# Performance work log

Measured on AMD Instinct MI355X. Metric: run time of the kernel, lower is better.

The kernel has to match this reference:

```python
import jax, jax.numpy as jnp
import numpy as np
import math

D_HEAD = 64
D_MODEL = 1024
N_HEADS = D_MODEL // D_HEAD
MAX_TOKENS = 2048
BATCH = 4
SEQ = 2048


def setup_inputs() -> dict:
    key = jax.random.key(0)
    k1, k2, k3, k4, k5 = jax.random.split(key, 5)
    residual_stream = jax.random.normal(k1, (BATCH, SEQ, D_MODEL), dtype=jnp.float32)
    # kaiming_normal_ (fan_in = d_model for [head, d_model, d_head] with default mode)
    std_qkv = math.sqrt(2.0 / D_MODEL)
    weight_query = jax.random.normal(k2, (N_HEADS, D_MODEL, D_HEAD), dtype=jnp.float32) * std_qkv
    weight_key = jax.random.normal(k3, (N_HEADS, D_MODEL, D_HEAD), dtype=jnp.float32) * std_qkv
    weight_value = jax.random.normal(k4, (N_HEADS, D_MODEL, D_HEAD), dtype=jnp.float32) * std_qkv
    # xavier_normal_ for [d_model, d_model]
    std_out = math.sqrt(2.0 / (D_MODEL + D_MODEL))
    weight_out = jax.random.normal(k5, (D_MODEL, D_MODEL), dtype=jnp.float32) * std_out
    return {
        "residual_stream": residual_stream,
        "weight_query": weight_query,
        "weight_key": weight_key,
        "weight_value": weight_value,
        "weight_out": weight_out,
    }


def reference(residual_stream, weight_query, weight_key, weight_value, weight_out):
    # residual_stream: [b, s, m]; weights: [h, m, d]
    q = jnp.einsum("bsm,hmd->bhsd", residual_stream, weight_query)
    k = jnp.einsum("bsm,hmd->bhsd", residual_stream, weight_key)
    v = jnp.einsum("bsm,hmd->bhsd", residual_stream, weight_value)
    scores = jnp.einsum("bhqd,bhkd->bhqk", q, k) / math.sqrt(D_HEAD)  # [b,h,s,s]
    n = scores.shape[-1]
    causal = jnp.tril(jnp.ones((n, n), dtype=bool))
    scores = jnp.where(causal, scores, -jnp.inf)
    attn = jax.nn.softmax(scores, axis=-1)
    out = jnp.einsum("bhqk,bhkd->bhqd", attn, v)  # [b,h,s,d]
    b, h, s, d = out.shape
    concat = out.transpose(0, 2, 1, 3).reshape(b, s, h * d)  # [b,s,m]
    return jnp.einsum("bsm,mn->bsn", concat, weight_out)
```

## Files before the change

### kernel.cpp

```cpp
#include <hip/hip_runtime.h>
#include <hip/hip_bf16.h>
#include <math.h>

#define BATCH 4
#define SEQ   2048
#define DM    1024
#define NH    16
#define DH    64

#define QSCALE 0.1803368801111204f

typedef __bf16 bf16x8 __attribute__((ext_vector_type(8)));
typedef __bf16 bf16x4 __attribute__((ext_vector_type(4)));
typedef float  f32x4  __attribute__((ext_vector_type(4)));

typedef const __attribute__((address_space(1))) unsigned int guint;
typedef __attribute__((address_space(3)))       unsigned int luint;

__device__ __forceinline__ void async16(const __bf16* g, __bf16* l) {
    __builtin_amdgcn_global_load_lds((guint*)g, (luint*)l, 16, 0, 0);
}

__device__ __forceinline__ float fast_exp2(float x) {
#if __has_builtin(__builtin_amdgcn_exp2f)
    return __builtin_amdgcn_exp2f(x);
#else
    float r; asm("v_exp_f32 %0, %1" : "=v"(r) : "v"(x)); return r;
#endif
}
__device__ __forceinline__ float fast_rcp(float x) {
#if __has_builtin(__builtin_amdgcn_rcpf)
    return __builtin_amdgcn_rcpf(x);
#else
    float r; asm("v_rcp_f32 %0, %1" : "=v"(r) : "v"(x)); return r;
#endif
}

__device__ __forceinline__ bf16x8 load8f(const float* __restrict__ base, size_t idx) {
    const float4 a = *(const float4*)(base + idx);
    const float4 b = *(const float4*)(base + idx + 4);
    bf16x8 r;
    r[0] = (__bf16)a.x; r[1] = (__bf16)a.y; r[2] = (__bf16)a.z; r[3] = (__bf16)a.w;
    r[4] = (__bf16)b.x; r[5] = (__bf16)b.y; r[6] = (__bf16)b.z; r[7] = (__bf16)b.w;
    return r;
}

__global__ __launch_bounds__(256)
void xconv_kernel(const float* __restrict__ X, __bf16* __restrict__ Xb)
{
    size_t idx = ((size_t)blockIdx.x * 256 + threadIdx.x) * 8;
    *(bf16x8*)&Xb[idx] = load8f(X, idx);
}

__global__ __launch_bounds__(256)
void wtrans_kernel(const float* __restrict__ src, __bf16* __restrict__ dst,
                   int K, int N)
{
    const int k0 = blockIdx.x * 64;
    const int n0 = blockIdx.y * 64;
    src += (size_t)blockIdx.z * K * N;
    dst += (size_t)blockIdx.z * K * N;

    __shared__ __bf16 T[64][65];
    const int t = threadIdx.x;

#pragma unroll
    for (int i = 0; i < 4; ++i) {
        int row = i * 16 + (t >> 4);
        int col = (t & 15) * 4;
        float4 v = *(const float4*)&src[(size_t)(k0 + row) * N + n0 + col];
        T[col + 0][row] = (__bf16)v.x;
        T[col + 1][row] = (__bf16)v.y;
        T[col + 2][row] = (__bf16)v.z;
        T[col + 3][row] = (__bf16)v.w;
    }
    __syncthreads();
#pragma unroll
    for (int i = 0; i < 4; ++i) {
        int n  = i * 16 + (t >> 4);
        int kc = (t & 15) * 4;
        bf16x4 v;
        v[0] = T[n][kc + 0]; v[1] = T[n][kc + 1];
        v[2] = T[n][kc + 2]; v[3] = T[n][kc + 3];
        *(bf16x4*)&dst[(size_t)(n0 + n) * K + k0 + kc] = v;
    }
}

__global__ __launch_bounds__(256)
void qkv_kernel(const __bf16* __restrict__ Xb,
                const __bf16* __restrict__ Wqt,
                const __bf16* __restrict__ Wkt,
                const __bf16* __restrict__ Wvt,
                __bf16* __restrict__ Qo,
                __bf16* __restrict__ Ko,
                __bf16* __restrict__ Vto)
{
    const int rowTile = blockIdx.x;
    const int h       = blockIdx.y;
    const size_t woff = (size_t)h * DH * DM;

    __shared__ __align__(16) __bf16 As[128 * 32];
    __shared__ __align__(16) __bf16 Bq[64 * 32];
    __shared__ __align__(16) __bf16 Bk[64 * 32];
    __shared__ __align__(16) __bf16 Bv[64 * 32];

    const int t    = threadIdx.x;
    const int wave = t >> 6;
    const int lane = t & 63;
    const int l15  = lane & 15;
    const int quad = lane >> 4;

    f32x4 aq[2][4], ak[2][4], av[2][4];
#pragma unroll
    for (int s = 0; s < 2; ++s)
#pragma unroll
        for (int i = 0; i < 4; ++i) {
            aq[s][i] = (f32x4){0.f, 0.f, 0.f, 0.f};
            ak[s][i] = (f32x4){0.f, 0.f, 0.f, 0.f};
            av[s][i] = (f32x4){0.f, 0.f, 0.f, 0.f};
        }

    const int r0 = rowTile * 128;
    const int lrow = lane >> 2;
    const int lcol = (lane & 3) * 8;

    for (int k0 = 0; k0 < DM; k0 += 32) {
        __syncthreads();
#pragma unroll
        for (int c = 0; c < 2; ++c) {
            const int rb = wave * 32 + c * 16;
            async16(&Xb[(size_t)(r0 + rb + lrow) * DM + k0 + lcol], &As[rb * 32]);
        }
        {
            const int rb = wave * 16;
            async16(&Wqt[woff + (size_t)(rb + lrow) * DM + k0 + lcol], &Bq[rb * 32]);
            async16(&Wkt[woff + (size_t)(rb + lrow) * DM + k0 + lcol], &Bk[rb * 32]);
            async16(&Wvt[woff + (size_t)(rb + lrow) * DM + k0 + lcol], &Bv[rb * 32]);
        }
        __syncthreads();

        bf16x8 a0 = *(const bf16x8*)&As[(wave * 16 + l15) * 32 + quad * 8];
        bf16x8 a1 = *(const bf16x8*)&As[(64 + wave * 16 + l15) * 32 + quad * 8];
#pragma unroll
        for (int ct = 0; ct < 4; ++ct) {
            bf16x8 bq = *(const bf16x8*)&Bq[(ct * 16 + l15) * 32 + quad * 8];
            aq[0][ct] = __builtin_amdgcn_mfma_f32_16x16x32_bf16(a0, bq, aq[0][ct], 0, 0, 0);
            aq[1][ct] = __builtin_amdgcn_mfma_f32_16x16x32_bf16(a1, bq, aq[1][ct], 0, 0, 0);
            bf16x8 bk = *(const bf16x8*)&Bk[(ct * 16 + l15) * 32 + quad * 8];
            ak[0][ct] = __builtin_amdgcn_mfma_f32_16x16x32_bf16(a0, bk, ak[0][ct], 0, 0, 0);
            ak[1][ct] = __builtin_amdgcn_mfma_f32_16x16x32_bf16(a1, bk, ak[1][ct], 0, 0, 0);
            bf16x8 bv = *(const bf16x8*)&Bv[(ct * 16 + l15) * 32 + quad * 8];
            av[0][ct] = __builtin_amdgcn_mfma_f32_16x16x32_bf16(a0, bv, av[0][ct], 0, 0, 0);
            av[1][ct] = __builtin_amdgcn_mfma_f32_16x16x32_bf16(a1, bv, av[1][ct], 0, 0, 0);
        }
    }

#pragma unroll
    for (int st = 0; st < 2; ++st) {
        const int rbase = r0 + st * 64 + wave * 16 + quad * 4;
        const int b = rbase >> 11;
        const int s = rbase & (SEQ - 1);
        const size_t bh = (size_t)(b * NH + h);
#pragma unroll
        for (int ct = 0; ct < 4; ++ct) {
            const int d = ct * 16 + l15;
#pragma unroll
            for (int reg = 0; reg < 4; ++reg) {
                Qo[(bh * SEQ + s + reg) * DH + d] = (__bf16)(aq[st][ct][reg] * QSCALE);
                Ko[(bh * SEQ + s + reg) * DH + d] = (__bf16)ak[st][ct][reg];
            }
            bf16x4 vv;
            vv[0] = (__bf16)av[st][ct][0]; vv[1] = (__bf16)av[st][ct][1];
            vv[2] = (__bf16)av[st][ct][2]; vv[3] = (__bf16)av[st][ct][3];
            *(bf16x4*)&Vto[(bh * DH + d) * SEQ + s] = vv;
        }
    }
}

__global__ __launch_bounds__(256)
void attn_kernel(const __bf16* __restrict__ Q,
                 const __bf16* __restrict__ K,
                 const __bf16* __restrict__ Vt,
                 __bf16* __restrict__ Cat)
{
    const int x   = blockIdx.x;
    const int qtA = x;
    const int qtB = 31 - x;
    const int bh  = blockIdx.y;
    const int b   = bh >> 4;
    const int h   = bh & 15;

    const __bf16* Qg  = Q  + (size_t)bh * SEQ * DH;
    const __bf16* Kg  = K  + (size_t)bh * SEQ * DH;
    const __bf16* Vtg = Vt + (size_t)bh * DH * SEQ;

    __shared__ __align__(16) __bf16 Ks[64 * 72];
    __shared__ __align__(16) __bf16 Vs[64 * 72];
    __shared__ __align__(16) __bf16 Ps[64 * 72];

    const int t    = threadIdx.x;
    const int wave = t >> 6;
    const int lane = t & 63;
    const int l15  = lane & 15;
    const int quad = lane >> 4;

    bf16x8 qfA[2], qfB[2];
    {
        const size_t rA = (size_t)(qtA * 64 + wave * 16 + l15);
        qfA[0] = *(const bf16x8*)&Qg[rA * DH + quad * 8];
        qfA[1] = *(const bf16x8*)&Qg[rA * DH + 32 + quad * 8];
        const size_t rB = (size_t)(qtB * 64 + wave * 16 + l15);
        qfB[0] = *(const bf16x8*)&Qg[rB * DH + quad * 8];
        qfB[1] = *(const bf16x8*)&Qg[rB * DH + 32 + quad * 8];
    }

    bf16x8 ones;
#pragma unroll
    for (int j = 0; j < 8; ++j) ones[j] = (__bf16)1.0f;

    f32x4 oA[4], oB[4], olA, olB;
#pragma unroll
    for (int ct = 0; ct < 4; ++ct) {
        oA[ct] = (f32x4){0.f, 0.f, 0.f, 0.f};
        oB[ct] = (f32x4){0.f, 0.f, 0.f, 0.f};
    }
    olA = (f32x4){0.f, 0.f, 0.f, 0.f};
    olB = (f32x4){0.f, 0.f, 0.f, 0.f};

    const int srow0 = t >> 3;
    const int scol  = (t & 7) * 8;
    bf16x8 kreg[2], vreg[2];
#pragma unroll
    for (int i = 0; i < 2; ++i) {
        int row = srow0 + i * 32;
        kreg[i] = *(const bf16x8*)&Kg[(size_t)row * DH + scol];
        vreg[i] = *(const bf16x8*)&Vtg[(size_t)row * SEQ + scol];
    }

    auto half_step = [&](const bf16x8* qf, f32x4* o, f32x4& ol, bool diag) {
        f32x4 sc[4];
#pragma unroll
        for (int ct = 0; ct < 4; ++ct) {
            sc[ct] = (f32x4){0.f, 0.f, 0.f, 0.f};
            bf16x8 b0 = *(const bf16x8*)&Ks[(ct * 16 + l15) * 72 + quad * 8];
            sc[ct] = __builtin_amdgcn_mfma_f32_16x16x32_bf16(qf[0], b0, sc[ct], 0, 0, 0);
            bf16x8 b1 = *(const bf16x8*)&Ks[(ct * 16 + l15) * 72 + 32 + quad * 8];
            sc[ct] = __builtin_amdgcn_mfma_f32_16x16x32_bf16(qf[1], b1, sc[ct], 0, 0, 0);
        }
        if (diag) {
#pragma unroll
            for (int ct = 0; ct < 4; ++ct)
#pragma unroll
                for (int r = 0; r < 4; ++r) {
                    int qr = wave * 16 + quad * 4 + r;
                    int kc = ct * 16 + l15;
                    if (kc > qr) sc[ct][r] = -INFINITY;
                }
        }
#pragma unroll
        for (int ct = 0; ct < 4; ++ct)
#pragma unroll
            for (int r = 0; r < 4; ++r)
                sc[ct][r] = fast_exp2(sc[ct][r]);

#pragma unroll
        for (int ct = 0; ct < 4; ++ct)
#pragma unroll
            for (int r = 0; r < 4; ++r)
                Ps[(wave * 16 + quad * 4 + r) * 72 + ct * 16 + l15] =
                    (__bf16)sc[ct][r];

        bf16x8 af0 = *(const bf16x8*)&Ps[(wave * 16 + l15) * 72 + quad * 8];
        bf16x8 af1 = *(const bf16x8*)&Ps[(wave * 16 + l15) * 72 + 32 + quad * 8];

#pragma unroll
        for (int ct = 0; ct < 4; ++ct) {
            bf16x8 v0 = *(const bf16x8*)&Vs[(ct * 16 + l15) * 72 + quad * 8];
            o[ct] = __builtin_amdgcn_mfma_f32_16x16x32_bf16(af0, v0, o[ct], 0, 0, 0);
            bf16x8 v1 = *(const bf16x8*)&Vs[(ct * 16 + l15) * 72 + 32 + quad * 8];
            o[ct] = __builtin_amdgcn_mfma_f32_16x16x32_bf16(af1, v1, o[ct], 0, 0, 0);
        }
        ol = __builtin_amdgcn_mfma_f32_16x16x32_bf16(af0, ones, ol, 0, 0, 0);
        ol = __builtin_amdgcn_mfma_f32_16x16x32_bf16(af1, ones, ol, 0, 0, 0);
    };

    for (int kt = 0; kt <= qtB; ++kt) {
        __syncthreads();
#pragma unroll
        for (int i = 0; i < 2; ++i) {
            int row = srow0 + i * 32;
            *(bf16x8*)&Ks[row * 72 + scol] = kreg[i];
            *(bf16x8*)&Vs[row * 72 + scol] = vreg[i];
        }
        __syncthreads();

        {
            const int kvn = (kt < qtB ? kt + 1 : kt) * 64;
#pragma unroll
            for (int i = 0; i < 2; ++i) {
                int row = srow0 + i * 32;
                kreg[i] = *(const bf16x8*)&Kg[(size_t)(kvn + row) * DH + scol];
                vreg[i] = *(const bf16x8*)&Vtg[(size_t)row * SEQ + kvn + scol];
            }
        }

        half_step(qfB, oB, olB, kt == qtB);
        if (kt <= qtA)
            half_step(qfA, oA, olA, kt == qtA);
    }

#pragma unroll
    for (int ct = 0; ct < 4; ++ct)
#pragma unroll
        for (int r = 0; r < 4; ++r) {
            int rr = wave * 16 + quad * 4 + r;
            int sA = qtA * 64 + rr;
            int sB = qtB * 64 + rr;
            Cat[((size_t)(b * SEQ + sA)) * DM + h * DH + ct * 16 + l15] =
                (__bf16)(oA[ct][r] * fast_rcp(olA[r]));
            Cat[((size_t)(b * SEQ + sB)) * DM + h * DH + ct * 16 + l15] =
                (__bf16)(oB[ct][r] * fast_rcp(olB[r]));
        }
}

__global__ __launch_bounds__(256)
void oproj_kernel(const __bf16* __restrict__ A,
                  const __bf16* __restrict__ Wot,
                  float* __restrict__ C)
{
    const int rowTile = blockIdx.x;
    const int colTile = blockIdx.y;
    const int r0 = rowTile * 128;
    const int n0 = colTile * 128;

    __shared__ __align__(16) __bf16 As[128 * 32];
    __shared__ __align__(16) __bf16 Bs[128 * 32];

    const int t    = threadIdx.x;
    const int wave = t >> 6;
    const int lane = t & 63;
    const int l15  = lane & 15;
    const int quad = lane >> 4;

    f32x4 acc[2][8];
#pragma unroll
    for (int s = 0; s < 2; ++s)
#pragma unroll
        for (int i = 0; i < 8; ++i) acc[s][i] = (f32x4){0.f, 0.f, 0.f, 0.f};

    const int lrow = lane >> 2;
    const int lcol = (lane & 3) * 8;

    for (int k0 = 0; k0 < DM; k0 += 32) {
        __syncthreads();
#pragma unroll
        for (int c = 0; c < 2; ++c) {
            const int rb = wave * 32 + c * 16;
            async16(&A  [(size_t)(r0 + rb + lrow) * DM + k0 + lcol], &As[rb * 32]);
            async16(&Wot[(size_t)(n0 + rb + lrow) * DM + k0 + lcol], &Bs[rb * 32]);
        }
        __syncthreads();

        bf16x8 a0 = *(const bf16x8*)&As[(wave * 16 + l15) * 32 + quad * 8];
        bf16x8 a1 = *(const bf16x8*)&As[(64 + wave * 16 + l15) * 32 + quad * 8];
#pragma unroll
        for (int ct = 0; ct < 8; ++ct) {
            bf16x8 bb = *(const bf16x8*)&Bs[(ct * 16 + l15) * 32 + quad * 8];
            acc[0][ct] = __builtin_amdgcn_mfma_f32_16x16x32_bf16(a0, bb, acc[0][ct], 0, 0, 0);
            acc[1][ct] = __builtin_amdgcn_mfma_f32_16x16x32_bf16(a1, bb, acc[1][ct], 0, 0, 0);
        }
    }

#pragma unroll
    for (int st = 0; st < 2; ++st)
#pragma unroll
        for (int ct = 0; ct < 8; ++ct)
#pragma unroll
            for (int reg = 0; reg < 4; ++reg) {
                int r = r0 + st * 64 + wave * 16 + quad * 4 + reg;
                int n = n0 + ct * 16 + l15;
                C[(size_t)r * DM + n] = acc[st][ct][reg];
            }
}

extern "C" void kernel_launch(void* const* d_in, const int* in_sizes, int n_in,
                              void* d_out, int out_size, void* d_ws, size_t ws_size,
                              hipStream_t stream)
{
    (void)in_sizes; (void)n_in; (void)out_size; (void)ws_size;
    const float* X  = (const float*)d_in[0];
    const float* Wq = (const float*)d_in[1];
    const float* Wk = (const float*)d_in[2];
    const float* Wv = (const float*)d_in[3];
    const float* Wo = (const float*)d_in[4];
    float* out = (float*)d_out;

    char* ws = (char*)d_ws;
    const size_t wqkv_b = (size_t)NH * DM * DH * sizeof(__bf16);
    const size_t wo_b   = (size_t)DM * DM * sizeof(__bf16);
    const size_t big_b  = (size_t)BATCH * NH * SEQ * DH * sizeof(__bf16);
    __bf16* Wqt = (__bf16*)(ws);
    __bf16* Wkt = (__bf16*)(ws + wqkv_b);
    __bf16* Wvt = (__bf16*)(ws + 2 * wqkv_b);
    __bf16* Wot = (__bf16*)(ws + 3 * wqkv_b);
    __bf16* Qb  = (__bf16*)(ws + 3 * wqkv_b + wo_b);
    __bf16* Kb  = (__bf16*)(ws + 3 * wqkv_b + wo_b + big_b);
    __bf16* Vtb = (__bf16*)(ws + 3 * wqkv_b + wo_b + 2 * big_b);
    __bf16* Cat = (__bf16*)(ws + 3 * wqkv_b + wo_b + 3 * big_b);
    __bf16* Xb  = (__bf16*)(ws + 3 * wqkv_b + wo_b + 4 * big_b);

    xconv_kernel<<<dim3(4096), 256, 0, stream>>>(X, Xb);
    wtrans_kernel<<<dim3(16, 1, 16), 256, 0, stream>>>(Wq, Wqt, DM, DH);
    wtrans_kernel<<<dim3(16, 1, 16), 256, 0, stream>>>(Wk, Wkt, DM, DH);
    wtrans_kernel<<<dim3(16, 1, 16), 256, 0, stream>>>(Wv, Wvt, DM, DH);
    wtrans_kernel<<<dim3(16, 16, 1), 256, 0, stream>>>(Wo, Wot, DM, DM);
    qkv_kernel<<<dim3(64, 16), 256, 0, stream>>>(Xb, Wqt, Wkt, Wvt, Qb, Kb, Vtb);
    attn_kernel<<<dim3(16, 64), 256, 0, stream>>>(Qb, Kb, Vtb, Cat);
    oproj_kernel<<<dim3(64, 8), 256, 0, stream>>>(Cat, Wot, out);
}
```

Before: 281.6 us.

## Interleave both query tiles' attention steps and merge QKV weight transposes

The attention inner loop now computes scores for both query tiles (A and B) together, sharing each K and V fragment load between them. Each tile gets its own half of an enlarged P buffer, so the MFMA chains for the two tiles can interleave and hide latency. Separately, the three Q/K/V weight-transpose launches become one kernel, which saves launch overhead. The cost is more register pressure from holding two sets of score tiles, plus twice the P shared memory.

```diff
diff --git a/kernel.cpp b/kernel.cpp
--- a/kernel.cpp
+++ b/kernel.cpp
@@ -53,13 +53,51 @@
 }
 
 __global__ __launch_bounds__(256)
+void wtrans3_kernel(const float* __restrict__ Wq,
+                    const float* __restrict__ Wk,
+                    const float* __restrict__ Wv,
+                    __bf16* __restrict__ Wqt,
+                    __bf16* __restrict__ Wkt,
+                    __bf16* __restrict__ Wvt)
+{
+    const int z = blockIdx.z;
+    const int m = z >> 4;
+    const int h = z & 15;
+    const float* src = (m == 0 ? Wq : m == 1 ? Wk : Wv) + (size_t)h * DM * DH;
+    __bf16*      dst = (m == 0 ? Wqt : m == 1 ? Wkt : Wvt) + (size_t)h * DH * DM;
+    const int k0 = blockIdx.x * 64;
+
+    __shared__ __bf16 T[64][65];
+    const int t = threadIdx.x;
+
+#pragma unroll
+    for (int i = 0; i < 4; ++i) {
+        int row = i * 16 + (t >> 4);
+        int col = (t & 15) * 4;
+        float4 v = *(const float4*)&src[(size_t)(k0 + row) * DH + col];
+        T[col + 0][row] = (__bf16)v.x;
+        T[col + 1][row] = (__bf16)v.y;
+        T[col + 2][row] = (__bf16)v.z;
+        T[col + 3][row] = (__bf16)v.w;
+    }
+    __syncthreads();
+#pragma unroll
+    for (int i = 0; i < 4; ++i) {
+        int n  = i * 16 + (t >> 4);
+        int kc = (t & 15) * 4;
+        bf16x4 v;
+        v[0] = T[n][kc + 0]; v[1] = T[n][kc + 1];
+        v[2] = T[n][kc + 2]; v[3] = T[n][kc + 3];
+        *(bf16x4*)&dst[(size_t)n * DM + k0 + kc] = v;
+    }
+}
+
+__global__ __launch_bounds__(256)
 void wtrans_kernel(const float* __restrict__ src, __bf16* __restrict__ dst,
                    int K, int N)
 {
     const int k0 = blockIdx.x * 64;
     const int n0 = blockIdx.y * 64;
-    src += (size_t)blockIdx.z * K * N;
-    dst += (size_t)blockIdx.z * K * N;
 
     __shared__ __bf16 T[64][65];
     const int t = threadIdx.x;
@@ -196,7 +234,7 @@
 
     __shared__ __align__(16) __bf16 Ks[64 * 72];
     __shared__ __align__(16) __bf16 Vs[64 * 72];
-    __shared__ __align__(16) __bf16 Ps[64 * 72];
+    __shared__ __align__(16) __bf16 Ps[128 * 72];
 
     const int t    = threadIdx.x;
     const int wave = t >> 6;
@@ -237,53 +275,6 @@
         vreg[i] = *(const bf16x8*)&Vtg[(size_t)row * SEQ + scol];
     }
 
-    auto half_step = [&](const bf16x8* qf, f32x4* o, f32x4& ol, bool diag) {
-        f32x4 sc[4];
-#pragma unroll
-        for (int ct = 0; ct < 4; ++ct) {
-            sc[ct] = (f32x4){0.f, 0.f, 0.f, 0.f};
-            bf16x8 b0 = *(const bf16x8*)&Ks[(ct * 16 + l15) * 72 + quad * 8];
-            sc[ct] = __builtin_amdgcn_mfma_f32_16x16x32_bf16(qf[0], b0, sc[ct], 0, 0, 0);
-            bf16x8 b1 = *(const bf16x8*)&Ks[(ct * 16 + l15) * 72 + 32 + quad * 8];
-            sc[ct] = __builtin_amdgcn_mfma_f32_16x16x32_bf16(qf[1], b1, sc[ct], 0, 0, 0);
-        }
-        if (diag) {
-#pragma unroll
-            for (int ct = 0; ct < 4; ++ct)
-#pragma unroll
-                for (int r = 0; r < 4; ++r) {
-                    int qr = wave * 16 + quad * 4 + r;
-                    int kc = ct * 16 + l15;
-                    if (kc > qr) sc[ct][r] = -INFINITY;
-                }
-        }
-#pragma unroll
-        for (int ct = 0; ct < 4; ++ct)
-#pragma unroll
-            for (int r = 0; r < 4; ++r)
-                sc[ct][r] = fast_exp2(sc[ct][r]);
-
-#pragma unroll
-        for (int ct = 0; ct < 4; ++ct)
-#pragma unroll
-            for (int r = 0; r < 4; ++r)
-                Ps[(wave * 16 + quad * 4 + r) * 72 + ct * 16 + l15] =
-                    (__bf16)sc[ct][r];
-
-        bf16x8 af0 = *(const bf16x8*)&Ps[(wave * 16 + l15) * 72 + quad * 8];
-        bf16x8 af1 = *(const bf16x8*)&Ps[(wave * 16 + l15) * 72 + 32 + quad * 8];
-
-#pragma unroll
-        for (int ct = 0; ct < 4; ++ct) {
-            bf16x8 v0 = *(const bf16x8*)&Vs[(ct * 16 + l15) * 72 + quad * 8];
-            o[ct] = __builtin_amdgcn_mfma_f32_16x16x32_bf16(af0, v0, o[ct], 0, 0, 0);
-            bf16x8 v1 = *(const bf16x8*)&Vs[(ct * 16 + l15) * 72 + 32 + quad * 8];
-            o[ct] = __builtin_amdgcn_mfma_f32_16x16x32_bf16(af1, v1, o[ct], 0, 0, 0);
-        }
-        ol = __builtin_amdgcn_mfma_f32_16x16x32_bf16(af0, ones, ol, 0, 0, 0);
-        ol = __builtin_amdgcn_mfma_f32_16x16x32_bf16(af1, ones, ol, 0, 0, 0);
-    };
-
     for (int kt = 0; kt <= qtB; ++kt) {
         __syncthreads();
 #pragma unroll
@@ -304,9 +295,84 @@
             }
         }
 
-        half_step(qfB, oB, olB, kt == qtB);
-        if (kt <= qtA)
-            half_step(qfA, oA, olA, kt == qtA);
+        const bool aAct = (kt <= qtA);
+
+        f32x4 scB[4], scA[4];
+#pragma unroll
+        for (int ct = 0; ct < 4; ++ct) {
+            scB[ct] = (f32x4){0.f, 0.f, 0.f, 0.f};
+            scA[ct] = (f32x4){0.f, 0.f, 0.f, 0.f};
+            bf16x8 b0 = *(const bf16x8*)&Ks[(ct * 16 + l15) * 72 + quad * 8];
+            bf16x8 b1 = *(const bf16x8*)&Ks[(ct * 16 + l15) * 72 + 32 + quad * 8];
+            scB[ct] = __builtin_amdgcn_mfma_f32_16x16x32_bf16(qfB[0], b0, scB[ct], 0, 0, 0);
+            scB[ct] = __builtin_amdgcn_mfma_f32_16x16x32_bf16(qfB[1], b1, scB[ct], 0, 0, 0);
+            if (aAct) {
+                scA[ct] = __builtin_amdgcn_mfma_f32_16x16x32_bf16(qfA[0], b0, scA[ct], 0, 0, 0);
+                scA[ct] = __builtin_amdgcn_mfma_f32_16x16x32_bf16(qfA[1], b1, scA[ct], 0, 0, 0);
+            }
+        }
+
+        if (kt == qtB) {
+#pragma unroll
+            for (int ct = 0; ct < 4; ++ct)
+#pragma unroll
+                for (int r = 0; r < 4; ++r) {
+                    int qr = wave * 16 + quad * 4 + r;
+                    int kc = ct * 16 + l15;
+                    if (kc > qr) scB[ct][r] = -INFINITY;
+                }
+        }
+#pragma unroll
+        for (int ct = 0; ct < 4; ++ct)
+#pragma unroll
+            for (int r = 0; r < 4; ++r)
+                Ps[(64 + wave * 16 + quad * 4 + r) * 72 + ct * 16 + l15] =
+                    (__bf16)fast_exp2(scB[ct][r]);
+
+        if (aAct) {
+            if (kt == qtA) {
+#pragma unroll
+                for (int ct = 0; ct < 4; ++ct)
+#pragma unroll
+                    for (int r = 0; r < 4; ++r) {
+                        int qr = wave * 16 + quad * 4 + r;
+                        int kc = ct * 16 + l15;
+                        if (kc > qr) scA[ct][r] = -INFINITY;
+                    }
+            }
+#pragma unroll
+            for (int ct = 0; ct < 4; ++ct)
+#pragma unroll
+                for (int r = 0; r < 4; ++r)
+                    Ps[(wave * 16 + quad * 4 + r) * 72 + ct * 16 + l15] =
+                        (__bf16)fast_exp2(scA[ct][r]);
+        }
+
+        bf16x8 afB0 = *(const bf16x8*)&Ps[(64 + wave * 16 + l15) * 72 + quad * 8];
+        bf16x8 afB1 = *(const bf16x8*)&Ps[(64 + wave * 16 + l15) * 72 + 32 + quad * 8];
+        bf16x8 afA0, afA1;
+        if (aAct) {
+            afA0 = *(const bf16x8*)&Ps[(wave * 16 + l15) * 72 + quad * 8];
+            afA1 = *(const bf16x8*)&Ps[(wave * 16 + l15) * 72 + 32 + quad * 8];
+        }
+
+#pragma unroll
+        for (int ct = 0; ct < 4; ++ct) {
+            bf16x8 v0 = *(const bf16x8*)&Vs[(ct * 16 + l15) * 72 + quad * 8];
+            bf16x8 v1 = *(const bf16x8*)&Vs[(ct * 16 + l15) * 72 + 32 + quad * 8];
+            oB[ct] = __builtin_amdgcn_mfma_f32_16x16x32_bf16(afB0, v0, oB[ct], 0, 0, 0);
+            oB[ct] = __builtin_amdgcn_mfma_f32_16x16x32_bf16(afB1, v1, oB[ct], 0, 0, 0);
+            if (aAct) {
+                oA[ct] = __builtin_amdgcn_mfma_f32_16x16x32_bf16(afA0, v0, oA[ct], 0, 0, 0);
+                oA[ct] = __builtin_amdgcn_mfma_f32_16x16x32_bf16(afA1, v1, oA[ct], 0, 0, 0);
+            }
+        }
+        olB = __builtin_amdgcn_mfma_f32_16x16x32_bf16(afB0, ones, olB, 0, 0, 0);
+        olB = __builtin_amdgcn_mfma_f32_16x16x32_bf16(afB1, ones, olB, 0, 0, 0);
+        if (aAct) {
+            olA = __builtin_amdgcn_mfma_f32_16x16x32_bf16(afA0, ones, olA, 0, 0, 0);
+            olA = __builtin_amdgcn_mfma_f32_16x16x32_bf16(afA1, ones, olA, 0, 0, 0);
+        }
     }
 
 #pragma unroll
@@ -410,9 +476,7 @@
     __bf16* Xb  = (__bf16*)(ws + 3 * wqkv_b + wo_b + 4 * big_b);
 
     xconv_kernel<<<dim3(4096), 256, 0, stream>>>(X, Xb);
-    wtrans_kernel<<<dim3(16, 1, 16), 256, 0, stream>>>(Wq, Wqt, DM, DH);
-    wtrans_kernel<<<dim3(16, 1, 16), 256, 0, stream>>>(Wk, Wkt, DM, DH);
-    wtrans_kernel<<<dim3(16, 1, 16), 256, 0, stream>>>(Wv, Wvt, DM, DH);
+    wtrans3_kernel<<<dim3(16, 1, 48), 256, 0, stream>>>(Wq, Wk, Wv, Wqt, Wkt, Wvt);
     wtrans_kernel<<<dim3(16, 16, 1), 256, 0, stream>>>(Wo, Wot, DM, DM);
     qkv_kernel<<<dim3(64, 16), 256, 0, stream>>>(Xb, Wqt, Wkt, Wvt, Qb, Kb, Vtb);
     attn_kernel<<<dim3(16, 64), 256, 0, stream>>>(Qb, Kb, Vtb, Cat);
```

Result: no change. 280.9 us (-0.3%).
